# Kernel tuning notes

Measured on AMD Instinct MI355X. Metric: run time of the kernel, lower is better.

The kernel has to match this reference:

```python
import jax, jax.numpy as jnp
import numpy as np

B, M, D, H, FF = 2, 2048, 1024, 16, 2624
DH = D // H  # 64, power of 2 as required by the kernel
EPS = 1e-5
THETA = 10000.0


def setup_inputs() -> dict:
    key = jax.random.key(0)
    ks = jax.random.split(key, 12)
    hidden_states = jax.random.normal(ks[0], (B, M, D), dtype=jnp.float32)
    # padding mask: 1=valid, 0=pad; vary valid lengths per batch element
    lengths = jnp.array([M, 3 * M // 4], dtype=jnp.int32)
    attention_mask = (jnp.arange(M)[None, :] < lengths[:, None]).astype(jnp.int32)
    s = 0.02
    return {
        "hidden_states": hidden_states,
        "attention_mask": attention_mask,
        "ln1_w": jnp.ones((D,), jnp.float32),
        "ln1_b": jnp.zeros((D,), jnp.float32),
        "wqkv_w": s * jax.random.normal(ks[1], (3 * D, D), jnp.float32),
        "wqkv_b": jnp.zeros((3 * D,), jnp.float32),
        "wo_w": s * jax.random.normal(ks[2], (D, D), jnp.float32),
        "ln2_w": jnp.ones((D,), jnp.float32),
        "ln2_b": jnp.zeros((D,), jnp.float32),
        "wi_w": s * jax.random.normal(ks[3], (2 * FF, D), jnp.float32),
        "wo_mlp_w": s * jax.random.normal(ks[4], (D, FF), jnp.float32),
    }


def _layernorm(x, w, b):
    mu = jnp.mean(x, axis=-1, keepdims=True)
    var = jnp.mean(jnp.square(x - mu), axis=-1, keepdims=True)
    return (x - mu) * jax.lax.rsqrt(var + EPS) * w + b


def _rope(q, k):
    # q,k: [B,H,M,DH]; half-split RoPE (q1' = q1*c - q2*s; q2' = q1*s + q2*c)
    half = DH // 2
    inv_freq = 1.0 / (THETA ** (jnp.arange(0, DH, 2, dtype=jnp.float32) / DH))  # [half]
    freqs = jnp.arange(M, dtype=jnp.float32)[:, None] * inv_freq[None, :]      # [M, half]
    c = jnp.cos(freqs)[None, None]  # [1,1,M,half]
    s = jnp.sin(freqs)[None, None]
    q1, q2 = q[..., :half], q[..., half:]
    k1, k2 = k[..., :half], k[..., half:]
    q = jnp.concatenate([q1 * c - q2 * s, q1 * s + q2 * c], axis=-1)
    k = jnp.concatenate([k1 * c - k2 * s, k1 * s + k2 * c], axis=-1)
    return q, k


def reference(hidden_states, attention_mask, ln1_w, ln1_b, wqkv_w, wqkv_b,
              wo_w, ln2_w, ln2_b, wi_w, wo_mlp_w):
    x = hidden_states
    xn = _layernorm(x, ln1_w, ln1_b)
    qkv = (xn @ wqkv_w.T + wqkv_b).reshape(B, M, 3, H, DH)
    q, k, v = [jnp.transpose(qkv[:, :, i], (0, 2, 1, 3)) for i in range(3)]  # [B,H,M,DH]
    q, k = _rope(q, k)
    scale = 1.0 / np.sqrt(DH)
    scores = jnp.einsum("bhmd,bhnd->bhmn", q, k) * scale
    keep = (attention_mask > 0)[:, None, None, :]  # [B,1,1,M] key-padding mask
    scores = jnp.where(keep, scores, -jnp.inf)
    attn = jax.nn.softmax(scores, axis=-1)
    o = jnp.einsum("bhmn,bhnd->bhmd", attn, v)
    attn_out = jnp.transpose(o, (0, 2, 1, 3)).reshape(B, M, D)
    x = x + attn_out @ wo_w.T
    # ModernBERT GeGLU MLP
    h = _layernorm(x, ln2_w, ln2_b)
    g = h @ wi_w.T
    inp, gate = g[..., :FF], g[..., FF:]
    x = x + (jax.nn.gelu(inp, approximate=False) * gate) @ wo_mlp_w.T
    return x
```

## Files before the change

### kernel.cpp

```cpp
#include <hip/hip_runtime.h>
#include <hip/hip_bf16.h>
#include <math.h>

#define BB 2
#define MM 2048
#define DD 1024
#define HH 16
#define DHH 64
#define FF_ 2624
#define FFP 2688
#define TT (BB*MM)

typedef unsigned short u16;
typedef __attribute__((ext_vector_type(4))) unsigned short ushort4v;
typedef __attribute__((ext_vector_type(8))) short short8;
typedef __attribute__((ext_vector_type(4))) float floatx4;

#define SCALE2 0.18033688011112043f

#define WAITVM(N) asm volatile("s_waitcnt vmcnt(" #N ")" ::: "memory")
#define CFENCE()  asm volatile("" ::: "memory")

__device__ __forceinline__ u16 f2bf(float f) {
    __hip_bfloat16 h = __float2bfloat16(f);
    return *(u16*)&h;
}
__device__ __forceinline__ float bf2f(u16 u) {
    __hip_bfloat16 h; *(u16*)&h = u;
    return __bfloat162float(h);
}
__device__ __forceinline__ float gelu_exact(float x) {
    return 0.5f * x * (1.0f + erff(x * 0.70710678118654752f));
}
__device__ __forceinline__ void gload_lds16(const void* g, void* l) {
    __builtin_amdgcn_global_load_lds(
        (const __attribute__((address_space(1))) unsigned int*)g,
        (__attribute__((address_space(3))) unsigned int*)l, 16, 0, 0);
}

__device__ __forceinline__ int xcd_swizzle(int id, int nb) {
    if (nb & 7) return id;
    return (id & 7) * (nb >> 3) + (id >> 3);
}

__global__ void cvt_all(const float* __restrict__ wqkv, const float* __restrict__ wo,
                        const float* __restrict__ wi, const float* __restrict__ womlp,
                        u16* __restrict__ dqkv, u16* __restrict__ dwo,
                        u16* __restrict__ dinp, u16* __restrict__ dgate,
                        u16* __restrict__ dmlp, float2* __restrict__ tab) {
    int bid = blockIdx.x, tid = threadIdx.x;
    if (bid < 3072) {
        int i = (bid * 256 + tid) * 4;
        float4 v = *(const float4*)(wqkv + i);
        ushort4v o = {f2bf(v.x), f2bf(v.y), f2bf(v.z), f2bf(v.w)};
        *(ushort4v*)(dqkv + i) = o;
    } else if (bid < 4096) {
        int i = ((bid - 3072) * 256 + tid) * 4;
        float4 v = *(const float4*)(wo + i);
        ushort4v o = {f2bf(v.x), f2bf(v.y), f2bf(v.z), f2bf(v.w)};
        *(ushort4v*)(dwo + i) = o;
    } else if (bid < 4096 + 2 * FFP) {
        int seg = (bid - 4096) / FFP;
        int row = (bid - 4096) % FFP;
        u16* dst = seg ? dgate : dinp;
        const float* src = wi + (size_t)(seg ? FF_ : 0) * DD;
        int c = tid * 4;
        ushort4v o = {0, 0, 0, 0};
        if (row < FF_) {
            float4 v = *(const float4*)(src + (size_t)row * DD + c);
            o.x = f2bf(v.x); o.y = f2bf(v.y); o.z = f2bf(v.z); o.w = f2bf(v.w);
        }
        *(ushort4v*)(dst + (size_t)row * DD + c) = o;
    } else if (bid < 4096 + 2 * FFP + 1024) {
        int row = bid - 4096 - 2 * FFP;
        for (int c = tid * 4; c < FFP; c += 1024) {
            ushort4v o = {0, 0, 0, 0};
            if (c < FF_) {
                float4 v = *(const float4*)(womlp + (size_t)row * FF_ + c);
                o.x = f2bf(v.x); o.y = f2bf(v.y); o.z = f2bf(v.z); o.w = f2bf(v.w);
            }
            *(ushort4v*)(dmlp + (size_t)row * FFP + c) = o;
        }
    } else {
        int bq = bid - (4096 + 2 * FFP + 1024);
        int base = bq * 1024;
        for (int idx = tid; idx < 1024; idx += 256) {
            int e = base + idx;
            int mi = e >> 5, i = e & 31;
            float fr = (float)mi * powf(10000.0f, -(float)i / 32.0f);
            tab[e] = make_float2(cosf(fr), sinf(fr));
        }
    }
}

__global__ void ln_kernel(const float* __restrict__ x, const float* __restrict__ w,
                          const float* __restrict__ b, u16* __restrict__ out) {
    int row = blockIdx.x;
    int tid = threadIdx.x;
    const float4 v = ((const float4*)(x + (size_t)row * DD))[tid];
    float s  = v.x + v.y + v.z + v.w;
    float ss = v.x*v.x + v.y*v.y + v.z*v.z + v.w*v.w;
    #pragma unroll
    for (int o = 32; o > 0; o >>= 1) { s += __shfl_down(s, o); ss += __shfl_down(ss, o); }
    __shared__ float sbuf[4], ssbuf[4];
    int wid = tid >> 6;
    if ((tid & 63) == 0) { sbuf[wid] = s; ssbuf[wid] = ss; }
    __syncthreads();
    float st  = sbuf[0] + sbuf[1] + sbuf[2] + sbuf[3];
    float sst = ssbuf[0] + ssbuf[1] + ssbuf[2] + ssbuf[3];
    float mean = st * (1.0f / DD);
    float var  = sst * (1.0f / DD) - mean * mean;
    float rstd = rsqrtf(var + 1e-5f);
    const float4 wv = ((const float4*)w)[tid];
    const float4 bv = ((const float4*)b)[tid];
    ushort4v o;
    o.x = f2bf((v.x - mean) * rstd * wv.x + bv.x);
    o.y = f2bf((v.y - mean) * rstd * wv.y + bv.y);
    o.z = f2bf((v.z - mean) * rstd * wv.z + bv.z);
    o.w = f2bf((v.w - mean) * rstd * wv.w + bv.w);
    ((ushort4v*)(out + (size_t)row * DD))[tid] = o;
}


template<int MODE, bool OUT_BF16>
__global__ __launch_bounds__(256, 4)
void mfma_gemm64(const u16* __restrict__ A, const u16* __restrict__ W,
                 const float* __restrict__ bias, const void* __restrict__ add,
                 void* __restrict__ Cout, int N, int K) {
    __shared__ u16 As[3][128 * 32];
    __shared__ u16 Bs[3][64 * 32];
    int tid = threadIdx.x;
    int w = tid >> 6, lane = tid & 63;
    int q = lane >> 4, m = lane & 15;

    int nbx = gridDim.x;
    int id = xcd_swizzle(blockIdx.y * nbx + blockIdx.x, nbx * gridDim.y);
    int bx = id % nbx, by = id / nbx;
    int row0 = by * 128, col0 = bx * 64;
    int wm = (w >> 1) * 64, wn = (w & 1) * 32;

    floatx4 acc[4][2];
    #pragma unroll
    for (int i = 0; i < 4; i++)
        #pragma unroll
        for (int j = 0; j < 2; j++)
            acc[i][j] = (floatx4){0.f, 0.f, 0.f, 0.f};

    int lrow = lane >> 2;
    int lcg  = (lane & 3) ^ ((lrow >> 1) & 3);
    const u16* Ag = A + (size_t)(row0 + w * 32 + lrow) * K + lcg * 8;
    const u16* Bg = W + (size_t)(col0 + w * 16 + lrow) * K + lcg * 8;
    int NT = K >> 5;
    int slot8 = (q ^ ((m >> 1) & 3)) * 8;

    auto stage = [&](int t, int buf) {
        const u16* Aq = Ag + (size_t)t * 32;
        const u16* Bq = Bg + (size_t)t * 32;
        gload_lds16(Aq,                  &As[buf][(w * 32) * 32]);
        gload_lds16(Aq + (size_t)16 * K, &As[buf][(w * 32 + 16) * 32]);
        gload_lds16(Bq,                  &Bs[buf][(w * 16) * 32]);
    };
    stage(0, 0); stage(1, 1);

    int cur = 0;
    for (int t = 0; t < NT; ++t) {
        if (t + 2 < NT) {
            int nxt = cur + 2; if (nxt >= 3) nxt -= 3;
            stage(t + 2, nxt);
            WAITVM(6);
        } else if (t + 2 == NT) {
            WAITVM(3);
        } else {
            WAITVM(0);
        }
        __builtin_amdgcn_s_barrier();
        CFENCE();
        short8 af[4], bf[2];
        #pragma unroll
        for (int f = 0; f < 4; f++)
            af[f] = *(const short8*)&As[cur][(wm + f * 16 + m) * 32 + slot8];
        #pragma unroll
        for (int f = 0; f < 2; f++)
            bf[f] = *(const short8*)&Bs[cur][(wn + f * 16 + m) * 32 + slot8];
        __builtin_amdgcn_s_setprio(1);
        #pragma unroll
        for (int mf = 0; mf < 4; mf++)
            #pragma unroll
            for (int nf = 0; nf < 2; nf++)
                acc[mf][nf] = __builtin_amdgcn_mfma_f32_16x16x32_bf16(
                    af[mf], bf[nf], acc[mf][nf], 0, 0, 0);
        __builtin_amdgcn_s_setprio(0);
        if (t + 1 < NT) {
            __builtin_amdgcn_s_barrier();
            CFENCE();
        }
        cur = (cur + 1 == 3) ? 0 : cur + 1;
    }

    #pragma unroll
    for (int nf = 0; nf < 2; nf++) {
        int col = col0 + wn + nf * 16 + m;
        float bv = 0.f;
        if (MODE == 0 && bias) bv = bias[col];
        #pragma unroll
        for (int mf = 0; mf < 4; mf++) {
            #pragma unroll
            for (int r = 0; r < 4; r++) {
                int row = row0 + wm + mf * 16 + q * 4 + r;
                size_t idx = (size_t)row * N + col;
                float vacc = acc[mf][nf][r] + bv;
                if (MODE == 1) vacc += ((const float*)add)[idx];
                if (OUT_BF16) ((u16*)Cout)[idx] = f2bf(vacc);
                else          ((float*)Cout)[idx] = vacc;
            }
        }
    }
}

__global__ __launch_bounds__(256, 4)
void mfma_gemm_qkv(const u16* __restrict__ A, const u16* __restrict__ W,
                   const float* __restrict__ bias, const float2* __restrict__ tab,
                   u16* __restrict__ qb, u16* __restrict__ kb, u16* __restrict__ vtb) {
    __shared__ u16 As[3][128 * 32];
    __shared__ u16 Bs[3][64 * 32];
    int tid = threadIdx.x;
    int w = tid >> 6, lane = tid & 63;
    int q = lane >> 4, m = lane & 15;

    int nbx = gridDim.x;
    int id = xcd_swizzle(blockIdx.y * nbx + blockIdx.x, nbx * gridDim.y);
    int bx = id % nbx, by = id / nbx;
    int row0 = by * 128, col0 = bx * 64;
    int wm = w * 32;

    floatx4 acc[2][4];
    #pragma unroll
    for (int i = 0; i < 2; i++)
        #pragma unroll
        for (int j = 0; j < 4; j++)
            acc[i][j] = (floatx4){0.f, 0.f, 0.f, 0.f};

    int lrow = lane >> 2;
    int lcg  = (lane & 3) ^ ((lrow >> 1) & 3);
    const u16* Ag = A + (size_t)(row0 + w * 32 + lrow) * DD + lcg * 8;
    const u16* Bg = W + (size_t)(col0 + w * 16 + lrow) * DD + lcg * 8;
    const int NT = DD >> 5;
    int slot8 = (q ^ ((m >> 1) & 3)) * 8;

    auto stage = [&](int t, int buf) {
        const u16* Aq = Ag + (size_t)t * 32;
        const u16* Bq = Bg + (size_t)t * 32;
        gload_lds16(Aq,                   &As[buf][(w * 32) * 32]);
        gload_lds16(Aq + (size_t)16 * DD, &As[buf][(w * 32 + 16) * 32]);
        gload_lds16(Bq,                   &Bs[buf][(w * 16) * 32]);
    };
    stage(0, 0); stage(1, 1);

    int cur = 0;
    for (int t = 0; t < NT; ++t) {
        if (t + 2 < NT) {
            int nxt = cur + 2; if (nxt >= 3) nxt -= 3;
            stage(t + 2, nxt);
            WAITVM(6);
        } else if (t + 2 == NT) {
            WAITVM(3);
        } else {
            WAITVM(0);
        }
        __builtin_amdgcn_s_barrier();
        CFENCE();
        short8 af[2], bf[4];
        #pragma unroll
        for (int f = 0; f < 2; f++)
            af[f] = *(const short8*)&As[cur][(wm + f * 16 + m) * 32 + slot8];
        #pragma unroll
        for (int f = 0; f < 4; f++)
            bf[f] = *(const short8*)&Bs[cur][(f * 16 + m) * 32 + slot8];
        __builtin_amdgcn_s_setprio(1);
        #pragma unroll
        for (int mf = 0; mf < 2; mf++)
            #pragma unroll
            for (int nf = 0; nf < 4; nf++)
                acc[mf][nf] = __builtin_amdgcn_mfma_f32_16x16x32_bf16(
                    af[mf], bf[nf], acc[mf][nf], 0, 0, 0);
        __builtin_amdgcn_s_setprio(0);
        if (t + 1 < NT) {
            __builtin_amdgcn_s_barrier();
            CFENCE();
        }
        cur = (cur + 1 == 3) ? 0 : cur + 1;
    }

    int seg = col0 >> 6;
    int b   = row0 >> 11;
    int mi0 = (row0 & 2047) + wm;

    float b0[4];
    #pragma unroll
    for (int nf = 0; nf < 4; nf++) b0[nf] = bias[col0 + nf * 16 + m];

    if (seg < 32) {
        int hq = seg & 15;
        u16* dst = (seg < 16 ? qb : kb) + (size_t)(b * HH + hq) * MM * DHH;
        #pragma unroll
        for (int mf = 0; mf < 2; mf++) {
            #pragma unroll
            for (int r = 0; r < 4; r++) {
                int mi = mi0 + mf * 16 + q * 4 + r;
                float2 cs0 = tab[mi * 32 + m];
                float2 cs1 = tab[mi * 32 + 16 + m];
                float a0 = acc[mf][0][r] + b0[0];
                float a1 = acc[mf][1][r] + b0[1];
                float a2 = acc[mf][2][r] + b0[2];
                float a3 = acc[mf][3][r] + b0[3];
                size_t base = (size_t)mi * DHH;
                dst[base + m]      = f2bf(a0 * cs0.x - a2 * cs0.y);
                dst[base + 32 + m] = f2bf(a0 * cs0.y + a2 * cs0.x);
                dst[base + 16 + m] = f2bf(a1 * cs1.x - a3 * cs1.y);
                dst[base + 48 + m] = f2bf(a1 * cs1.y + a3 * cs1.x);
            }
        }
    } else {
        int hv = seg & 15;
        u16* dst = vtb + (size_t)(b * HH + hv) * DHH * MM;
        #pragma unroll
        for (int nf = 0; nf < 4; nf++) {
            int d = nf * 16 + m;
            #pragma unroll
            for (int mf = 0; mf < 2; mf++) {
                int mi = mi0 + mf * 16 + q * 4;
                ushort4v o;
                o.x = f2bf(acc[mf][nf][0] + b0[nf]);
                o.y = f2bf(acc[mf][nf][1] + b0[nf]);
                o.z = f2bf(acc[mf][nf][2] + b0[nf]);
                o.w = f2bf(acc[mf][nf][3] + b0[nf]);
                *(ushort4v*)(dst + (size_t)d * MM + mi) = o;
            }
        }
    }
}

__global__ __launch_bounds__(256, 3)
void mfma_gemm_glu(const u16* __restrict__ A, const u16* __restrict__ W1,
                   const u16* __restrict__ W2, u16* __restrict__ Cout) {
    __shared__ u16 As [3][128 * 32];
    __shared__ u16 B1s[3][64 * 32];
    __shared__ u16 B2s[3][64 * 32];
    int tid = threadIdx.x;
    int w = tid >> 6, lane = tid & 63;
    int q = lane >> 4, m = lane & 15;

    int nbx = gridDim.x;
    int id = xcd_swizzle(blockIdx.y * nbx + blockIdx.x, nbx * gridDim.y);
    int bx = id % nbx, by = id / nbx;
    int row0 = by * 128, col0 = bx * 64;
    int wm = (w >> 1) * 64, wn = (w & 1) * 32;

    floatx4 acc1[4][2], acc2[4][2];
    #pragma unroll
    for (int i = 0; i < 4; i++)
        #pragma unroll
        for (int j = 0; j < 2; j++) {
            acc1[i][j] = (floatx4){0.f, 0.f, 0.f, 0.f};
            acc2[i][j] = (floatx4){0.f, 0.f, 0.f, 0.f};
        }

    int lrow = lane >> 2;
    int lcg  = (lane & 3) ^ ((lrow >> 1) & 3);
    const u16* Ag  = A  + (size_t)(row0 + w * 32 + lrow) * DD + lcg * 8;
    const u16* B1g = W1 + (size_t)(col0 + w * 16 + lrow) * DD + lcg * 8;
    const u16* B2g = W2 + (size_t)(col0 + w * 16 + lrow) * DD + lcg * 8;
    const int NT = DD >> 5;
    int slot8 = (q ^ ((m >> 1) & 3)) * 8;

    auto stage = [&](int t, int buf) {
        const u16* Aq  = Ag  + (size_t)t * 32;
        const u16* B1q = B1g + (size_t)t * 32;
        const u16* B2q = B2g + (size_t)t * 32;
        gload_lds16(Aq,                   &As [buf][(w * 32) * 32]);
        gload_lds16(Aq + (size_t)16 * DD, &As [buf][(w * 32 + 16) * 32]);
        gload_lds16(B1q,                  &B1s[buf][(w * 16) * 32]);
        gload_lds16(B2q,                  &B2s[buf][(w * 16) * 32]);
    };
    stage(0, 0); stage(1, 1);

    int cur = 0;
    for (int t = 0; t < NT; ++t) {
        if (t + 2 < NT) {
            int nxt = cur + 2; if (nxt >= 3) nxt -= 3;
            stage(t + 2, nxt);
            WAITVM(8);
        } else if (t + 2 == NT) {
            WAITVM(4);
        } else {
            WAITVM(0);
        }
        __builtin_amdgcn_s_barrier();
        CFENCE();
        short8 af[4], b1f[2], b2f[2];
        #pragma unroll
        for (int f = 0; f < 4; f++)
            af[f] = *(const short8*)&As[cur][(wm + f * 16 + m) * 32 + slot8];
        #pragma unroll
        for (int f = 0; f < 2; f++) {
            b1f[f] = *(const short8*)&B1s[cur][(wn + f * 16 + m) * 32 + slot8];
            b2f[f] = *(const short8*)&B2s[cur][(wn + f * 16 + m) * 32 + slot8];
        }
        __builtin_amdgcn_s_setprio(1);
        #pragma unroll
        for (int mf = 0; mf < 4; mf++)
            #pragma unroll
            for (int nf = 0; nf < 2; nf++) {
                acc1[mf][nf] = __builtin_amdgcn_mfma_f32_16x16x32_bf16(
                    af[mf], b1f[nf], acc1[mf][nf], 0, 0, 0);
                acc2[mf][nf] = __builtin_amdgcn_mfma_f32_16x16x32_bf16(
                    af[mf], b2f[nf], acc2[mf][nf], 0, 0, 0);
            }
        __builtin_amdgcn_s_setprio(0);
        if (t + 1 < NT) {
            __builtin_amdgcn_s_barrier();
            CFENCE();
        }
        cur = (cur + 1 == 3) ? 0 : cur + 1;
    }

    #pragma unroll
    for (int nf = 0; nf < 2; nf++) {
        int col = col0 + wn + nf * 16 + m;
        #pragma unroll
        for (int mf = 0; mf < 4; mf++) {
            #pragma unroll
            for (int r = 0; r < 4; r++) {
                int row = row0 + wm + mf * 16 + q * 4 + r;
                Cout[(size_t)row * FFP + col] =
                    f2bf(gelu_exact(acc1[mf][nf][r]) * acc2[mf][nf][r]);
            }
        }
    }
}

__global__ __launch_bounds__(256, 4)
void flash_attn_mfma(const u16* __restrict__ q, const u16* __restrict__ k,
                     const u16* __restrict__ vt, const int* __restrict__ mask,
                     u16* __restrict__ out) {
    __shared__ __align__(16) u16 Ks[2][64 * 64];
    __shared__ __align__(16) u16 Vs[2][64 * 64];
    __shared__ __align__(16) u16 QP[64 * 64];

    int tid = threadIdx.x;
    int w = tid >> 6, lane = tid & 63;
    int quad = lane >> 4, m = lane & 15;
    int mt = blockIdx.x, h = blockIdx.y, b = blockIdx.z;
    int m0 = mt * 64;
    size_t bh = (size_t)(b * HH + h);
    const u16* qg  = q  + (bh * MM + m0) * DHH;
    const u16* kg  = k  + bh * MM * DHH;
    const u16* vtg = vt + bh * DHH * MM;
    int wr0 = w * 16;

    int lrow = lane >> 3, lcg = (lane & 7) ^ lrow;

    {
        const u16* Qg = qg + (size_t)(wr0 + lrow) * DHH + lcg * 8;
        gload_lds16(Qg,                     &QP[wr0 * 64]);
        gload_lds16(Qg + (size_t)8 * DHH,   &QP[(wr0 + 8) * 64]);
        const u16* Kg = kg + (size_t)(wr0 + lrow) * DHH + lcg * 8;
        gload_lds16(Kg,                     &Ks[0][wr0 * 64]);
        gload_lds16(Kg + (size_t)8 * DHH,   &Ks[0][(wr0 + 8) * 64]);
        const u16* Vg = vtg + (size_t)(wr0 + lrow) * MM + lcg * 8;
        gload_lds16(Vg,                     &Vs[0][wr0 * 64]);
        gload_lds16(Vg + (size_t)8 * MM,    &Vs[0][(wr0 + 8) * 64]);
    }
    WAITVM(4);
    CFENCE();

    short8 qf[2];
    #pragma unroll
    for (int ks = 0; ks < 2; ks++) {
        int slot = (ks * 4 + quad) ^ (m & 7);
        qf[ks] = *(const short8*)&QP[(wr0 + m) * 64 + slot * 8];
    }

    floatx4 O[4];
    #pragma unroll
    for (int df = 0; df < 4; df++) O[df] = (floatx4){0.f, 0.f, 0.f, 0.f};
    float lsum[4] = {};

    u16* Pw = &QP[wr0 * 64];

    for (int n0 = 0; n0 < MM; n0 += 64) {
        if (mask[b * MM + n0] == 0) break;
        int cur = (n0 >> 6) & 1;
        bool pre = (n0 + 64 < MM) && (mask[b * MM + n0 + 64] != 0);
        if (pre) {
            const u16* Kg = kg + (size_t)(n0 + 64 + wr0 + lrow) * DHH + lcg * 8;
            gload_lds16(Kg,                   &Ks[cur ^ 1][wr0 * 64]);
            gload_lds16(Kg + (size_t)8 * DHH, &Ks[cur ^ 1][(wr0 + 8) * 64]);
            const u16* Vg = vtg + (size_t)(wr0 + lrow) * MM + (n0 + 64) + lcg * 8;
            gload_lds16(Vg,                   &Vs[cur ^ 1][wr0 * 64]);
            gload_lds16(Vg + (size_t)8 * MM,  &Vs[cur ^ 1][(wr0 + 8) * 64]);
            WAITVM(4);
        } else {
            WAITVM(0);
        }
        __builtin_amdgcn_s_barrier();
        CFENCE();

        floatx4 S[4];
        #pragma unroll
        for (int nf = 0; nf < 4; nf++) S[nf] = (floatx4){0.f, 0.f, 0.f, 0.f};
        #pragma unroll
        for (int ks = 0; ks < 2; ks++) {
            short8 kf[4];
            #pragma unroll
            for (int nf = 0; nf < 4; nf++) {
                int slot = (ks * 4 + quad) ^ (m & 7);
                kf[nf] = *(const short8*)&Ks[cur][(nf * 16 + m) * 64 + slot * 8];
            }
            __builtin_amdgcn_s_setprio(1);
            #pragma unroll
            for (int nf = 0; nf < 4; nf++)
                S[nf] = __builtin_amdgcn_mfma_f32_16x16x32_bf16(
                    qf[ks], kf[nf], S[nf], 0, 0, 0);
            __builtin_amdgcn_s_setprio(0);
        }

        #pragma unroll
        for (int r = 0; r < 4; r++) {
            float s0 = exp2f(S[0][r] * SCALE2);
            float s1 = exp2f(S[1][r] * SCALE2);
            float s2 = exp2f(S[2][r] * SCALE2);
            float s3 = exp2f(S[3][r] * SCALE2);
            S[0][r] = s0; S[1][r] = s1; S[2][r] = s2; S[3][r] = s3;
            lsum[r] += (s0 + s1) + (s2 + s3);
        }

        #pragma unroll
        for (int nf = 0; nf < 4; nf++)
            #pragma unroll
            for (int r = 0; r < 4; r++) {
                int prow = quad * 4 + r;
                int pcol = nf * 16 + m;
                int slot = (pcol >> 3) ^ (prow & 7);
                Pw[prow * 64 + slot * 8 + (pcol & 7)] = f2bf(S[nf][r]);
            }

        #pragma unroll
        for (int ks = 0; ks < 2; ks++) {
            int slot = (ks * 4 + quad) ^ (m & 7);
            short8 pf = *(const short8*)&Pw[m * 64 + slot * 8];
            short8 vf[4];
            #pragma unroll
            for (int df = 0; df < 4; df++) {
                int d = df * 16 + m;
                vf[df] = *(const short8*)&Vs[cur][d * 64 + slot * 8];
            }
            __builtin_amdgcn_s_setprio(1);
            #pragma unroll
            for (int df = 0; df < 4; df++)
                O[df] = __builtin_amdgcn_mfma_f32_16x16x32_bf16(
                    pf, vf[df], O[df], 0, 0, 0);
            __builtin_amdgcn_s_setprio(0);
        }
        __builtin_amdgcn_s_barrier();
        CFENCE();
    }
    WAITVM(0);
    CFENCE();

    float inv[4];
    #pragma unroll
    for (int r = 0; r < 4; r++) {
        float s = lsum[r];
        #pragma unroll
        for (int o = 1; o < 16; o <<= 1) s += __shfl_xor(s, o);
        inv[r] = 1.0f / s;
    }
    #pragma unroll
    for (int df = 0; df < 4; df++) {
        int d = df * 16 + m;
        #pragma unroll
        for (int r = 0; r < 4; r++) {
            int row = m0 + wr0 + quad * 4 + r;
            out[((size_t)(b * MM) + row) * DD + h * DHH + d] =
                f2bf(O[df][r] * inv[r]);
        }
    }
}

extern "C" void kernel_launch(void* const* d_in, const int* in_sizes, int n_in,
                              void* d_out, int out_size, void* d_ws, size_t ws_size,
                              hipStream_t stream) {
    const float* hidden   = (const float*)d_in[0];
    const int*   mask     = (const int*)d_in[1];
    const float* ln1_w    = (const float*)d_in[2];
    const float* ln1_b    = (const float*)d_in[3];
    const float* wqkv_w   = (const float*)d_in[4];
    const float* wqkv_b   = (const float*)d_in[5];
    const float* wo_w     = (const float*)d_in[6];
    const float* ln2_w    = (const float*)d_in[7];
    const float* ln2_b    = (const float*)d_in[8];
    const float* wi_w     = (const float*)d_in[9];
    const float* wo_mlp_w = (const float*)d_in[10];
    float* out = (float*)d_out;

    char* ws = (char*)d_ws;
    u16* wqkv_bf  = (u16*)(ws);
    u16* wo_bf    = (u16*)(ws + 6291456);
    u16* wi_inp   = (u16*)(ws + 8388608);
    u16* wi_gate  = (u16*)(ws + 13893632);
    u16* womlp_bf = (u16*)(ws + 19398656);
    u16* xn       = (u16*)(ws + 24903680);
    float2* rtab  = (float2*)(ws + 33292288);
    u16* qb       = (u16*)(ws + 58458112);
    u16* kb       = (u16*)(ws + 66846720);
    u16* vtb      = (u16*)(ws + 75235328);
    u16* attn_out = (u16*)(ws + 83623936);
    u16* hb       = (u16*)(ws + 92012544);
    u16* act      = (u16*)(ws + 58458112);

    cvt_all<<<4096 + 2 * FFP + 1024 + 64, 256, 0, stream>>>(
        wqkv_w, wo_w, wi_w, wo_mlp_w, wqkv_bf, wo_bf, wi_inp, wi_gate, womlp_bf, rtab);
    ln_kernel<<<TT, 256, 0, stream>>>(hidden, ln1_w, ln1_b, xn);
    mfma_gemm_qkv<<<dim3(3 * DD / 64, TT / 128), 256, 0, stream>>>(
        xn, wqkv_bf, wqkv_b, rtab, qb, kb, vtb);
    flash_attn_mfma<<<dim3(MM / 64, HH, BB), 256, 0, stream>>>(qb, kb, vtb, mask, attn_out);
    mfma_gemm64<1, false><<<dim3(DD / 64, TT / 128), 256, 0, stream>>>(
        attn_out, wo_bf, nullptr, hidden, out, DD, DD);
    ln_kernel<<<TT, 256, 0, stream>>>(out, ln2_w, ln2_b, hb);
    mfma_gemm_glu<<<dim3(FFP / 64, TT / 128), 256, 0, stream>>>(
        hb, wi_inp, wi_gate, act);
    mfma_gemm64<1, false><<<dim3(DD / 64, TT / 128), 256, 0, stream>>>(
        act, womlp_bf, nullptr, out, out, DD, FFP);
}
```

Before: 370.8 us.

## Rewrite flash attention with 32x32 MFMA and register-resident P

```diff
diff --git a/kernel.cpp b/kernel.cpp
--- a/kernel.cpp
+++ b/kernel.cpp
@@ -15,6 +15,7 @@
 typedef __attribute__((ext_vector_type(4))) unsigned short ushort4v;
 typedef __attribute__((ext_vector_type(8))) short short8;
 typedef __attribute__((ext_vector_type(4))) float floatx4;
+typedef __attribute__((ext_vector_type(16))) float floatx16;
 
 #define SCALE2 0.18033688011112043f
 
@@ -36,6 +37,18 @@
     __builtin_amdgcn_global_load_lds(
         (const __attribute__((address_space(1))) unsigned int*)g,
         (__attribute__((address_space(3))) unsigned int*)l, 16, 0, 0);
+}
+__device__ __forceinline__ unsigned int cvt_pk_bf16(float a, float b) {
+    unsigned int r;
+    asm("v_cvt_pk_bf16_f32 %0, %1, %2" : "=v"(r) : "v"(a), "v"(b));
+    return r;
+}
+__device__ __forceinline__ short8 pack8(float a0, float a1, float a2, float a3,
+                                        float a4, float a5, float a6, float a7) {
+    union { unsigned int u[4]; short8 s; } r;
+    r.u[0] = cvt_pk_bf16(a0, a1); r.u[1] = cvt_pk_bf16(a2, a3);
+    r.u[2] = cvt_pk_bf16(a4, a5); r.u[3] = cvt_pk_bf16(a6, a7);
+    return r.s;
 }
 
 __device__ __forceinline__ int xcd_swizzle(int id, int nb) {
@@ -439,66 +452,65 @@
     }
 }
 
-__global__ __launch_bounds__(256, 4)
-void flash_attn_mfma(const u16* __restrict__ q, const u16* __restrict__ k,
-                     const u16* __restrict__ vt, const int* __restrict__ mask,
-                     u16* __restrict__ out) {
-    __shared__ __align__(16) u16 Ks[2][64 * 64];
-    __shared__ __align__(16) u16 Vs[2][64 * 64];
-    __shared__ __align__(16) u16 QP[64 * 64];
+__global__ __launch_bounds__(256, 2)
+void flash_attn_mfma32(const u16* __restrict__ qp, const u16* __restrict__ kp,
+                       const u16* __restrict__ vt, const int* __restrict__ mask,
+                       u16* __restrict__ out) {
+    __shared__ __align__(16) u16 Ks[2 * 64 * 64];
+    __shared__ __align__(16) u16 Vs[2 * 64 * 64];
 
     int tid = threadIdx.x;
     int w = tid >> 6, lane = tid & 63;
-    int quad = lane >> 4, m = lane & 15;
+    int col = lane & 31, hi = lane >> 5;
     int mt = blockIdx.x, h = blockIdx.y, b = blockIdx.z;
-    int m0 = mt * 64;
+    int m0 = mt * 128;
     size_t bh = (size_t)(b * HH + h);
-    const u16* qg  = q  + (bh * MM + m0) * DHH;
-    const u16* kg  = k  + bh * MM * DHH;
+    const u16* qg  = qp + (bh * MM + m0 + w * 32) * DHH;
+    const u16* kg  = kp + bh * MM * DHH;
     const u16* vtg = vt + bh * DHH * MM;
-    int wr0 = w * 16;
-
-    int lrow = lane >> 3, lcg = (lane & 7) ^ lrow;
-
-    {
-        const u16* Qg = qg + (size_t)(wr0 + lrow) * DHH + lcg * 8;
-        gload_lds16(Qg,                     &QP[wr0 * 64]);
-        gload_lds16(Qg + (size_t)8 * DHH,   &QP[(wr0 + 8) * 64]);
-        const u16* Kg = kg + (size_t)(wr0 + lrow) * DHH + lcg * 8;
-        gload_lds16(Kg,                     &Ks[0][wr0 * 64]);
-        gload_lds16(Kg + (size_t)8 * DHH,   &Ks[0][(wr0 + 8) * 64]);
-        const u16* Vg = vtg + (size_t)(wr0 + lrow) * MM + lcg * 8;
-        gload_lds16(Vg,                     &Vs[0][wr0 * 64]);
-        gload_lds16(Vg + (size_t)8 * MM,    &Vs[0][(wr0 + 8) * 64]);
-    }
-    WAITVM(4);
-    CFENCE();
-
-    short8 qf[2];
-    #pragma unroll
-    for (int ks = 0; ks < 2; ks++) {
-        int slot = (ks * 4 + quad) ^ (m & 7);
-        qf[ks] = *(const short8*)&QP[(wr0 + m) * 64 + slot * 8];
-    }
-
-    floatx4 O[4];
-    #pragma unroll
-    for (int df = 0; df < 4; df++) O[df] = (floatx4){0.f, 0.f, 0.f, 0.f};
-    float lsum[4] = {};
-
-    u16* Pw = &QP[wr0 * 64];
-
-    for (int n0 = 0; n0 < MM; n0 += 64) {
-        if (mask[b * MM + n0] == 0) break;
-        int cur = (n0 >> 6) & 1;
-        bool pre = (n0 + 64 < MM) && (mask[b * MM + n0 + 64] != 0);
-        if (pre) {
-            const u16* Kg = kg + (size_t)(n0 + 64 + wr0 + lrow) * DHH + lcg * 8;
-            gload_lds16(Kg,                   &Ks[cur ^ 1][wr0 * 64]);
-            gload_lds16(Kg + (size_t)8 * DHH, &Ks[cur ^ 1][(wr0 + 8) * 64]);
-            const u16* Vg = vtg + (size_t)(wr0 + lrow) * MM + (n0 + 64) + lcg * 8;
-            gload_lds16(Vg,                   &Vs[cur ^ 1][wr0 * 64]);
-            gload_lds16(Vg + (size_t)8 * MM,  &Vs[cur ^ 1][(wr0 + 8) * 64]);
+
+    int ntv = 0;
+    for (int n = 0; n < MM; n += 64) ntv += (mask[b * MM + n] != 0);
+
+    short8 qf[4];
+    #pragma unroll
+    for (int t = 0; t < 4; t++)
+        qf[t] = *(const short8*)(qg + (size_t)col * DHH + (2 * t + hi) * 8);
+
+    int lr = lane >> 3, lc = lane & 7;
+    int lcg = lc ^ lr;
+    int i0 = w * 16 + lr, i1 = i0 + 8;
+    int sg0 = (i0 & ~12) | ((i0 & 4) << 1) | ((i0 & 8) >> 1);
+    int sg1 = (i1 & ~12) | ((i1 & 4) << 1) | ((i1 & 8) >> 1);
+    const u16* Kg0 = kg + (size_t)sg0 * DHH + lcg * 8;
+    const u16* Kg1 = kg + (size_t)sg1 * DHH + lcg * 8;
+    const u16* Vg0 = vtg + (size_t)i0 * MM + lcg * 8;
+    const u16* Vg1 = vtg + (size_t)i1 * MM + lcg * 8;
+    u16* KL0 = Ks + (w * 16) * 64;
+    u16* KL1 = KL0 + 8 * 64;
+    u16* VL0 = Vs + (w * 16) * 64;
+    u16* VL1 = VL0 + 8 * 64;
+    const int BUFO = 64 * 64;
+
+    gload_lds16(Kg0, KL0); gload_lds16(Kg1, KL1);
+    gload_lds16(Vg0, VL0); gload_lds16(Vg1, VL1);
+
+    floatx16 O0, O1;
+    #pragma unroll
+    for (int r = 0; r < 16; r++) { O0[r] = 0.f; O1[r] = 0.f; }
+    float ls = 0.f;
+
+    int swz = (col & 7) * 8;
+
+    for (int it = 0; it < ntv; ++it) {
+        int cur = it & 1;
+        int co = cur * BUFO, po = (cur ^ 1) * BUFO;
+        if (it + 1 < ntv) {
+            size_t nk = (size_t)(it + 1) * 64;
+            gload_lds16(Kg0 + nk * DHH, KL0 + po);
+            gload_lds16(Kg1 + nk * DHH, KL1 + po);
+            gload_lds16(Vg0 + nk,       VL0 + po);
+            gload_lds16(Vg1 + nk,       VL1 + po);
             WAITVM(4);
         } else {
             WAITVM(0);
@@ -506,60 +518,42 @@
         __builtin_amdgcn_s_barrier();
         CFENCE();
 
-        floatx4 S[4];
-        #pragma unroll
-        for (int nf = 0; nf < 4; nf++) S[nf] = (floatx4){0.f, 0.f, 0.f, 0.f};
-        #pragma unroll
-        for (int ks = 0; ks < 2; ks++) {
-            short8 kf[4];
-            #pragma unroll
-            for (int nf = 0; nf < 4; nf++) {
-                int slot = (ks * 4 + quad) ^ (m & 7);
-                kf[nf] = *(const short8*)&Ks[cur][(nf * 16 + m) * 64 + slot * 8];
-            }
+        floatx16 P0, P1;
+        #pragma unroll
+        for (int r = 0; r < 16; r++) { P0[r] = 0.f; P1[r] = 0.f; }
+        #pragma unroll
+        for (int t = 0; t < 4; t++) {
+            int ck = (((2 * t + hi) * 8) ^ swz);
+            short8 kf0 = *(const short8*)&Ks[co + col * 64 + ck];
+            short8 kf1 = *(const short8*)&Ks[co + (32 + col) * 64 + ck];
             __builtin_amdgcn_s_setprio(1);
-            #pragma unroll
-            for (int nf = 0; nf < 4; nf++)
-                S[nf] = __builtin_amdgcn_mfma_f32_16x16x32_bf16(
-                    qf[ks], kf[nf], S[nf], 0, 0, 0);
+            P0 = __builtin_amdgcn_mfma_f32_32x32x16_bf16(kf0, qf[t], P0, 0, 0, 0);
+            P1 = __builtin_amdgcn_mfma_f32_32x32x16_bf16(kf1, qf[t], P1, 0, 0, 0);
             __builtin_amdgcn_s_setprio(0);
         }
 
         #pragma unroll
-        for (int r = 0; r < 4; r++) {
-            float s0 = exp2f(S[0][r] * SCALE2);
-            float s1 = exp2f(S[1][r] * SCALE2);
-            float s2 = exp2f(S[2][r] * SCALE2);
-            float s3 = exp2f(S[3][r] * SCALE2);
-            S[0][r] = s0; S[1][r] = s1; S[2][r] = s2; S[3][r] = s3;
-            lsum[r] += (s0 + s1) + (s2 + s3);
-        }
-
-        #pragma unroll
-        for (int nf = 0; nf < 4; nf++)
-            #pragma unroll
-            for (int r = 0; r < 4; r++) {
-                int prow = quad * 4 + r;
-                int pcol = nf * 16 + m;
-                int slot = (pcol >> 3) ^ (prow & 7);
-                Pw[prow * 64 + slot * 8 + (pcol & 7)] = f2bf(S[nf][r]);
-            }
-
-        #pragma unroll
-        for (int ks = 0; ks < 2; ks++) {
-            int slot = (ks * 4 + quad) ^ (m & 7);
-            short8 pf = *(const short8*)&Pw[m * 64 + slot * 8];
-            short8 vf[4];
-            #pragma unroll
-            for (int df = 0; df < 4; df++) {
-                int d = df * 16 + m;
-                vf[df] = *(const short8*)&Vs[cur][d * 64 + slot * 8];
-            }
+        for (int r = 0; r < 16; r++) {
+            float e0 = exp2f(P0[r] * SCALE2);
+            float e1 = exp2f(P1[r] * SCALE2);
+            P0[r] = e0; P1[r] = e1;
+            ls += e0 + e1;
+        }
+
+        short8 pa0 = pack8(P0[0], P0[1], P0[2],  P0[3],  P0[4],  P0[5],  P0[6],  P0[7]);
+        short8 pa1 = pack8(P0[8], P0[9], P0[10], P0[11], P0[12], P0[13], P0[14], P0[15]);
+        short8 pa2 = pack8(P1[0], P1[1], P1[2],  P1[3],  P1[4],  P1[5],  P1[6],  P1[7]);
+        short8 pa3 = pack8(P1[8], P1[9], P1[10], P1[11], P1[12], P1[13], P1[14], P1[15]);
+
+        #pragma unroll
+        for (int s = 0; s < 4; s++) {
+            int ck = (((2 * s + hi) * 8) ^ swz);
+            short8 vf0 = *(const short8*)&Vs[co + col * 64 + ck];
+            short8 vf1 = *(const short8*)&Vs[co + (32 + col) * 64 + ck];
+            short8 pas = (s == 0) ? pa0 : (s == 1) ? pa1 : (s == 2) ? pa2 : pa3;
             __builtin_amdgcn_s_setprio(1);
-            #pragma unroll
-            for (int df = 0; df < 4; df++)
-                O[df] = __builtin_amdgcn_mfma_f32_16x16x32_bf16(
-                    pf, vf[df], O[df], 0, 0, 0);
+            O0 = __builtin_amdgcn_mfma_f32_32x32x16_bf16(pas, vf0, O0, 0, 0, 0);
+            O1 = __builtin_amdgcn_mfma_f32_32x32x16_bf16(pas, vf1, O1, 0, 0, 0);
             __builtin_amdgcn_s_setprio(0);
         }
         __builtin_amdgcn_s_barrier();
@@ -568,23 +562,20 @@
     WAITVM(0);
     CFENCE();
 
-    float inv[4];
-    #pragma unroll
-    for (int r = 0; r < 4; r++) {
-        float s = lsum[r];
-        #pragma unroll
-        for (int o = 1; o < 16; o <<= 1) s += __shfl_xor(s, o);
-        inv[r] = 1.0f / s;
-    }
-    #pragma unroll
-    for (int df = 0; df < 4; df++) {
-        int d = df * 16 + m;
-        #pragma unroll
-        for (int r = 0; r < 4; r++) {
-            int row = m0 + wr0 + quad * 4 + r;
-            out[((size_t)(b * MM) + row) * DD + h * DHH + d] =
-                f2bf(O[df][r] * inv[r]);
-        }
+    ls += __shfl_xor(ls, 32);
+    float inv = 1.0f / ls;
+    float invr[16];
+    #pragma unroll
+    for (int r = 0; r < 16; r++) {
+        int crow = (r & 3) + 8 * (r >> 2) + 4 * hi;
+        invr[r] = __shfl(inv, crow, 64);
+    }
+    u16* ob = out + ((size_t)(b * MM) + m0 + w * 32) * DD + h * DHH;
+    #pragma unroll
+    for (int r = 0; r < 16; r++) {
+        int crow = (r & 3) + 8 * (r >> 2) + 4 * hi;
+        ob[(size_t)crow * DD + col]      = f2bf(O0[r] * invr[r]);
+        ob[(size_t)crow * DD + 32 + col] = f2bf(O1[r] * invr[r]);
     }
 }
 
@@ -624,7 +615,8 @@
     ln_kernel<<<TT, 256, 0, stream>>>(hidden, ln1_w, ln1_b, xn);
     mfma_gemm_qkv<<<dim3(3 * DD / 64, TT / 128), 256, 0, stream>>>(
         xn, wqkv_bf, wqkv_b, rtab, qb, kb, vtb);
-    flash_attn_mfma<<<dim3(MM / 64, HH, BB), 256, 0, stream>>>(qb, kb, vtb, mask, attn_out);
+    flash_attn_mfma32<<<dim3(MM / 128, HH, BB), 256, 0, stream>>>(
+        qb, kb, vtb, mask, attn_out);
     mfma_gemm64<1, false><<<dim3(DD / 64, TT / 128), 256, 0, stream>>>(
         attn_out, wo_bf, nullptr, hidden, out, DD, DD);
     ln_kernel<<<TT, 256, 0, stream>>>(out, ln2_w, ln2_b, hb);
```

After: 361.9 us. -2.4%, faster.
